# Optimization experiments

Hardware: AMD Instinct MI355X
Metric: run time of the kernel (lower is better)

Reference implementation:

```python
import jax, jax.numpy as jnp
import numpy as np

B, T, C = 4, 4096, 128

def setup_inputs() -> dict:
    key = jax.random.key(0)
    k1, k2, k3, k4 = jax.random.split(key, 4)
    x = jax.random.normal(k1, (B, T, C), dtype=jnp.float32)
    s = 1.0 / np.sqrt(C)
    Wq = jax.random.normal(k2, (C, C), dtype=jnp.float32) * s
    Wk = jax.random.normal(k3, (C, C), dtype=jnp.float32) * s
    Wv = jax.random.normal(k4, (C, C), dtype=jnp.float32) * s
    return {"x": x, "Wq": Wq, "Wk": Wk, "Wv": Wv}

def reference(x, Wq, Wk, Wv):
    # nn.Linear(bias=False): y = x @ W.T
    q = jnp.einsum('btc,dc->btd', x, Wq)
    k = jnp.einsum('btc,dc->btd', x, Wk)
    v = jnp.einsum('btc,dc->btd', x, Wv)
    scale = 1.0 / jnp.sqrt(jnp.asarray(x.shape[-1], x.dtype))
    att = jnp.einsum('btd,bsd->bts', q, k) * scale  # [B,T,T]
    causal = jnp.tril(jnp.ones((x.shape[1], x.shape[1]), dtype=bool))
    att = jnp.where(causal[None, :, :], att, -jnp.inf)
    w = jax.nn.softmax(att, axis=-1)
    # dropout p=0.0 -> identity
    out = jnp.einsum('bts,bsd->btd', w, v)
    return out
```

## Files before the change

### kernel.cpp

```cpp
#include <hip/hip_runtime.h>
#include <hip/hip_bf16.h>
#include <math.h>

#define T_SEQ 4096
#define C_DIM 128
#define B_SZ  4

typedef __attribute__((ext_vector_type(8))) short short8;
typedef __attribute__((ext_vector_type(4))) short short4v;
typedef __attribute__((ext_vector_type(4))) float f32x4;

__device__ __forceinline__ short f2bf(float f) {
    union { float fv; unsigned u; } v; v.fv = f;
    unsigned r = v.u + 0x7fff + ((v.u >> 16) & 1);
    return (short)(r >> 16);
}

__device__ __forceinline__ unsigned pk_bf16(float a, float b) {
    union { __hip_bfloat162 h2; unsigned u; } c;
    c.h2 = __float22bfloat162_rn(make_float2(a, b));
    return c.u;
}

__device__ __forceinline__ short8 load_f32x8_bf16(const float* p) {
    const float4* q = (const float4*)p;
    float4 a = q[0], b = q[1];
    short8 r;
    r[0] = f2bf(a.x); r[1] = f2bf(a.y); r[2] = f2bf(a.z); r[3] = f2bf(a.w);
    r[4] = f2bf(b.x); r[5] = f2bf(b.y); r[6] = f2bf(b.z); r[7] = f2bf(b.w);
    return r;
}

__device__ __forceinline__ void async_cp16(const short* g, short* l) {
    __builtin_amdgcn_global_load_lds(
        (const __attribute__((address_space(1))) unsigned int*)g,
        (__attribute__((address_space(3))) unsigned int*)l, 16, 0, 0);
}

__global__ __launch_bounds__(256) void qkv_proj(
    const float* __restrict__ x, const float* __restrict__ Wq,
    const float* __restrict__ Wk, const float* __restrict__ Wv,
    short* __restrict__ Q, short* __restrict__ Kf, short* __restrict__ Vf)
{
    __shared__ short8 Wl[2048];

    const int tid  = threadIdx.x;
    const int lane = tid & 63;
    const int ln15 = lane & 15;
    const int quad = lane >> 4;
    const int mat  = blockIdx.x >> 7;
    const int rt   = (blockIdx.x & 127) * 4 + (tid >> 6);
    const int m0   = rt * 32;

    const float* W = (mat == 0) ? Wq : (mat == 1) ? Wk : Wv;

#pragma unroll
    for (int it = 0; it < 8; ++it) {
        int i = tid + it * 256;
        int n = i >> 4, kc = i & 15;
        short8 v = load_f32x8_bf16(W + n * C_DIM + kc * 8);
        Wl[((n >> 4) * 4 + (kc >> 2)) * 64 + (kc & 3) * 16 + (n & 15)] = v;
    }

    short8 afr[2][4];
#pragma unroll
    for (int ms = 0; ms < 2; ++ms) {
        const float* xrow = x + (size_t)(m0 + ms * 16 + ln15) * C_DIM + quad * 8;
#pragma unroll
        for (int ks = 0; ks < 4; ++ks)
            afr[ms][ks] = load_f32x8_bf16(xrow + ks * 32);
    }

    __syncthreads();

    const float scale = (mat == 0) ? (0.08838834764831845f * 1.4426950408889634f)
                                   : 1.0f;
    const int b  = m0 >> 12;
    const int tl = m0 & 4095;

#pragma unroll
    for (int nt = 0; nt < 8; ++nt) {
        f32x4 acc0 = {0.f, 0.f, 0.f, 0.f};
        f32x4 acc1 = {0.f, 0.f, 0.f, 0.f};
#pragma unroll
        for (int ks = 0; ks < 4; ++ks) {
            short8 bfr = Wl[(nt * 4 + ks) * 64 + lane];
            if (mat == 2) {
                acc0 = __builtin_amdgcn_mfma_f32_16x16x32_bf16(afr[0][ks], bfr, acc0, 0, 0, 0);
                acc1 = __builtin_amdgcn_mfma_f32_16x16x32_bf16(afr[1][ks], bfr, acc1, 0, 0, 0);
            } else {
                acc0 = __builtin_amdgcn_mfma_f32_16x16x32_bf16(bfr, afr[0][ks], acc0, 0, 0, 0);
                acc1 = __builtin_amdgcn_mfma_f32_16x16x32_bf16(bfr, afr[1][ks], acc1, 0, 0, 0);
            }
        }
        if (mat == 0) {
            short4v s0, s1;
#pragma unroll
            for (int r = 0; r < 4; ++r) { s0[r] = f2bf(acc0[r] * scale); s1[r] = f2bf(acc1[r] * scale); }
            *(short4v*)&Q[(size_t)(m0 + ln15) * C_DIM + nt * 16 + quad * 4]      = s0;
            *(short4v*)&Q[(size_t)(m0 + 16 + ln15) * C_DIM + nt * 16 + quad * 4] = s1;
        } else if (mat == 1) {
            short4v s0, s1;
#pragma unroll
            for (int r = 0; r < 4; ++r) { s0[r] = f2bf(acc0[r]); s1[r] = f2bf(acc1[r]); }
            const int ks     = nt >> 1;
            const int quad_k = (nt & 1) * 2 + (quad >> 1);
            const int j0     = (quad & 1) * 4;
            {
                const int A0 = (tl >> 4) & 3;
                const int rd = tl >> 6;
                const int kt = (A0 >> 1) * 2 + ((ln15 >> 2) & 1);
                const int ar = (((A0 & 1) << 1) | ((ln15 >> 3) & 1)) * 4 + (ln15 & 3);
                size_t a = ((size_t)b << 19) + (size_t)rd * 8192
                         + (kt * 4 + ks) * 512 + quad_k * 128 + ar * 8 + j0;
                *(short4v*)&Kf[a] = s0;
            }
            {
                const int A1 = ((tl >> 4) + 1) & 3;
                const int rd = (tl + 16) >> 6;
                const int kt = (A1 >> 1) * 2 + ((ln15 >> 2) & 1);
                const int ar = (((A1 & 1) << 1) | ((ln15 >> 3) & 1)) * 4 + (ln15 & 3);
                size_t a = ((size_t)b << 19) + (size_t)rd * 8192
                         + (kt * 4 + ks) * 512 + quad_k * 128 + ar * 8 + j0;
                *(short4v*)&Kf[a] = s1;
            }
        } else {
            const int kvc = tl >> 5;
            short4v s0, s1;
#pragma unroll
            for (int r = 0; r < 4; ++r) { s0[r] = f2bf(acc0[r]); s1[r] = f2bf(acc1[r]); }
            short* vbase = Vf + (((size_t)(b * 128 + kvc) * 8 + nt) << 9);
            *(short4v*)&vbase[((quad >> 1) * 16 + ln15) * 8 + (quad & 1) * 4]       = s0;
            *(short4v*)&vbase[(((quad >> 1) + 2) * 16 + ln15) * 8 + (quad & 1) * 4] = s1;
        }
    }
}


#define QK8(KARR, SA, SB)                                                    \
    _Pragma("unroll")                                                        \
    for (int ks = 0; ks < 4; ++ks) {                                         \
      SA = __builtin_amdgcn_mfma_f32_16x16x32_bf16(KARR[ks],   qf[ks], SA, 0,0,0); \
      SB = __builtin_amdgcn_mfma_f32_16x16x32_bf16(KARR[4+ks], qf[ks], SB, 0,0,0); \
    }

#define SM8(SA, SB, PA)                                                      \
    {                                                                        \
      float p0 = __builtin_amdgcn_exp2f(SA[0] - 16.f);                       \
      float p1 = __builtin_amdgcn_exp2f(SA[1] - 16.f);                       \
      float p2 = __builtin_amdgcn_exp2f(SA[2] - 16.f);                       \
      float p3 = __builtin_amdgcn_exp2f(SA[3] - 16.f);                       \
      float p4 = __builtin_amdgcn_exp2f(SB[0] - 16.f);                       \
      float p5 = __builtin_amdgcn_exp2f(SB[1] - 16.f);                       \
      float p6 = __builtin_amdgcn_exp2f(SB[2] - 16.f);                       \
      float p7 = __builtin_amdgcn_exp2f(SB[3] - 16.f);                       \
      l_i += ((p0 + p1) + (p2 + p3)) + ((p4 + p5) + (p6 + p7));              \
      PA.u[0] = pk_bf16(p0, p1); PA.u[1] = pk_bf16(p2, p3);                  \
      PA.u[2] = pk_bf16(p4, p5); PA.u[3] = pk_bf16(p6, p7);                  \
    }

#define MASK8(SA, SB, CC)                                                    \
    if (32 * (CC) + 31 > Rw) {                                               \
      const int qcol = Rw + ln15;                                            \
      const int kb   = 32 * (CC) + quad * 8;                                 \
      _Pragma("unroll")                                                      \
      for (int rr = 0; rr < 4; ++rr) {                                       \
        if (kb + rr > qcol)     SA[rr] = -INFINITY;                          \
        if (kb + 4 + rr > qcol) SB[rr] = -INFINITY;                          \
      }                                                                      \
    }

#define PV8(VB_, OFF, PA)                                                    \
    _Pragma("unroll")                                                        \
    for (int dt = 0; dt < 8; ++dt) {                                         \
      short8 vfr = *(const short8*)&(VB_)[(OFF) + dt * 512 + lane * 8];      \
      acc[dt] = __builtin_amdgcn_mfma_f32_16x16x32_bf16(PA.s8, vfr,          \
                                                        acc[dt], 0, 0, 0);   \
    }

#define CHUNK2(KB_, VB_, T0)                                                 \
  {                                                                          \
    const int cc1 = qq + 4 * (T0) + 4;                                       \
    short8 kfr0[8];                                                          \
    _Pragma("unroll")                                                        \
    for (int j = 0; j < 8; ++j)                                              \
      kfr0[j] = *(const short8*)&(KB_)[j * 512 + lane * 8];                  \
    __builtin_amdgcn_s_setprio(1);                                           \
    f32x4 Sa0 = {0.f,0.f,0.f,0.f}, Sb0 = {0.f,0.f,0.f,0.f};                  \
    QK8(kfr0, Sa0, Sb0)                                                      \
    short8 kfr1[8];                                                          \
    _Pragma("unroll")                                                        \
    for (int j = 0; j < 8; ++j)                                              \
      kfr1[j] = *(const short8*)&(KB_)[4096 + j * 512 + lane * 8];           \
    f32x4 Sa1 = {0.f,0.f,0.f,0.f}, Sb1 = {0.f,0.f,0.f,0.f};                  \
    QK8(kfr1, Sa1, Sb1)                                                      \
    union { unsigned u[4]; short8 s8; } pa0, pa1;                            \
    SM8(Sa0, Sb0, pa0)                                                       \
    PV8(VB_, 0, pa0)                                                         \
    MASK8(Sa1, Sb1, cc1)                                                     \
    SM8(Sa1, Sb1, pa1)                                                       \
    PV8(VB_, 4096, pa1)                                                      \
    __builtin_amdgcn_s_setprio(0);                                           \
  }

#define CHUNK1(KB_, VB_, T0)                                                 \
  {                                                                          \
    const int cc0 = qq + 4 * (T0);                                           \
    short8 kfr0[8];                                                          \
    _Pragma("unroll")                                                        \
    for (int j = 0; j < 8; ++j)                                              \
      kfr0[j] = *(const short8*)&(KB_)[j * 512 + lane * 8];                  \
    __builtin_amdgcn_s_setprio(1);                                           \
    f32x4 Sa0 = {0.f,0.f,0.f,0.f}, Sb0 = {0.f,0.f,0.f,0.f};                  \
    QK8(kfr0, Sa0, Sb0)                                                      \
    MASK8(Sa0, Sb0, cc0)                                                     \
    union { unsigned u[4]; short8 s8; } pa0;                                 \
    SM8(Sa0, Sb0, pa0)                                                       \
    PV8(VB_, 0, pa0)                                                         \
    __builtin_amdgcn_s_setprio(0);                                           \
  }

#define ROUND(KC, VC, KN, VN, R)                                             \
  {                                                                          \
                       \
    asm volatile("s_waitcnt vmcnt(0)" ::: "memory");                         \
    __builtin_amdgcn_sched_barrier(0);                                       \
    __builtin_amdgcn_s_barrier();                                            \
    __builtin_amdgcn_sched_barrier(0);                                       \
          \
    {                                                                        \
      const int slot = (w >> 1) & 1;                                         \
      const int tS   = 2 * (R) + 2 + slot;                                   \
      if (tS <= gg) {                                                        \
        const int hw = w & 1;                                                \
        const short* src = ((w < 4) ? Kb : Vb)                               \
                         + (size_t)(qq + 4 * tS) * 4096 + hw * 2048;         \
        short* dst = ((w < 4) ? (KN) : (VN)) + slot * 4096 + hw * 2048;      \
        _Pragma("unroll")                                                    \
        for (int i = 0; i < 4; ++i)                                          \
          async_cp16(src + i * 512 + lane * 8, dst + i * 512);               \
      }                                                                      \
    }                                                                        \
    const int t0 = 2 * (R);                                                  \
    const bool a1 = (t0 + 1 <= gg) && (32 * (qq + 4 * t0 + 4) <= Rw + 15);   \
    const bool a0 = (t0 <= gg) && (32 * (qq + 4 * t0) <= Rw + 15);           \
    if (a1)      CHUNK2(KC, VC, t0)                                          \
    else if (a0) CHUNK1(KC, VC, t0)                                          \
  }

__global__ __launch_bounds__(512, 2) void flash_attn(
    const short* __restrict__ Q, const short* __restrict__ Kf,
    const short* __restrict__ Vf, float* __restrict__ part,
    float* __restrict__ lpart)
{
    __shared__ short Kld0[8192];
    __shared__ short Kld1[8192];
    __shared__ short Vld0[8192];
    __shared__ short Vld1[8192];

    const int tid  = threadIdx.x;
    const int w    = tid >> 6;
    const int lane = tid & 63;
    const int ln15 = lane & 15;
    const int quad = lane >> 4;
    const int bid  = blockIdx.x;

    const int u     = bid & 255;
    const int ph    = bid >> 8;
    const int xg    = u >> 3;
    const int gg    = ph ? xg : (31 - xg);
    const int combo = (ph << 3) | (u & 7);
    const int b     = combo >> 2;
    const int qq    = combo & 3;

    const int Rw   = 128 * gg + 16 * w;
    const int nrounds = (gg >> 1) + 1;

    const short* Qb = Q  + ((size_t)b << 19);
    const short* Kb = Kf + ((size_t)b << 19);
    const short* Vb = Vf + ((size_t)b << 19);

    short8 qf[4];
    {
        const short* qrow = Qb + (size_t)(Rw + ln15) * C_DIM + quad * 8;
#pragma unroll
        for (int ks = 0; ks < 4; ++ks)
            qf[ks] = *(const short8*)(qrow + ks * 32);
    }

    f32x4 acc[8];
#pragma unroll
    for (int dt = 0; dt < 8; ++dt)
        acc[dt] = (f32x4){0.f, 0.f, 0.f, 0.f};
    float l_i = 0.f;

    {
        const int slot = (w >> 1) & 1;
        const int tS   = slot;
        if (tS <= gg) {
            const int hw = w & 1;
            const short* src = ((w < 4) ? Kb : Vb)
                             + (size_t)(qq + 4 * tS) * 4096 + hw * 2048;
            short* dst = ((w < 4) ? Kld0 : Vld0) + slot * 4096 + hw * 2048;
#pragma unroll
            for (int i = 0; i < 4; ++i)
                async_cp16(src + i * 512 + lane * 8, dst + i * 512);
        }
    }

    int r = 0;
    while (true) {
        ROUND(Kld0, Vld0, Kld1, Vld1, r);
        if (++r >= nrounds) break;
        ROUND(Kld1, Vld1, Kld0, Vld0, r);
        if (++r >= nrounds) break;
    }

    l_i += __shfl_xor(l_i, 16);
    l_i += __shfl_xor(l_i, 32);

    float* pp = part + (((size_t)(qq * 4 + b)) * 4096 + Rw) * 128;
#pragma unroll
    for (int dt = 0; dt < 8; ++dt)
#pragma unroll
        for (int rr = 0; rr < 4; ++rr)
            pp[(quad * 4 + rr) * 128 + dt * 16 + ln15] = acc[dt][rr];
    if (quad == 0)
        lpart[(size_t)(qq * 4 + b) * 4096 + Rw + ln15] = l_i;
}

__global__ __launch_bounds__(256) void combine(
    const float* __restrict__ part, const float* __restrict__ lpart,
    float* __restrict__ out)
{
    const int tid = threadIdx.x;
    const int bid = blockIdx.x;

#pragma unroll
    for (int i = 0; i < 8; ++i) {
        int f4  = bid * 2048 + i * 256 + tid;
        int c4  = f4 & 31;
        int row = f4 >> 5;
        int b   = row >> 12;
        int trow = row & 4095;

        float4 p = make_float4(0.f, 0.f, 0.f, 0.f);
        float  l = 0.f;
#pragma unroll
        for (int q = 0; q < 4; ++q) {
            size_t base = (((size_t)(q * 4 + b)) * 4096 + trow) * 128 + c4 * 4;
            float4 pq = *(const float4*)&part[base];
            p.x += pq.x; p.y += pq.y; p.z += pq.z; p.w += pq.w;
            l += lpart[(size_t)(q * 4 + b) * 4096 + trow];
        }
        float li = 1.0f / l;
        float4 v;
        v.x = p.x * li; v.y = p.y * li; v.z = p.z * li; v.w = p.w * li;
        ((float4*)out)[f4] = v;
    }
}

extern "C" void kernel_launch(void* const* d_in, const int* in_sizes, int n_in,
                              void* d_out, int out_size, void* d_ws, size_t ws_size,
                              hipStream_t stream) {
    const float* x  = (const float*)d_in[0];
    const float* Wq = (const float*)d_in[1];
    const float* Wk = (const float*)d_in[2];
    const float* Wv = (const float*)d_in[3];
    float* out = (float*)d_out;

    const size_t elems = (size_t)B_SZ * T_SEQ * C_DIM;
    short* Q  = (short*)d_ws;
    short* Kf = Q  + elems;
    short* Vf = Kf + elems;
    float* part  = (float*)(Vf + elems);
    float* lpart = part + (size_t)16 * 4096 * 128;

    hipLaunchKernelGGL(qkv_proj, dim3(384), dim3(256), 0, stream,
                       x, Wq, Wk, Wv, Q, Kf, Vf);
    hipLaunchKernelGGL(flash_attn, dim3(512), dim3(512), 0, stream,
                       Q, Kf, Vf, part, lpart);
    hipLaunchKernelGGL(combine, dim3(256), dim3(256), 0, stream,
                       part, lpart, out);
}
```

Before: 108.0 us.

## Have each wave process 32 query rows to reuse K/V fragments across two tiles

Block size drops from 8 waves to 4, and each wave now owns 32 query rows (two 16-row tiles) instead of 16. Every K and V fragment read from LDS feeds MFMAs for both tiles, which halves LDS read traffic per unit of compute. The async copy work is redistributed so 2 waves load K and 2 load V, each covering full 4096-element slots. In exchange, accumulator registers per wave double and there are fewer waves available to hide latency, which may hurt occupancy. Masking is now applied to both chunks instead of being selectively skipped.

```diff
diff --git a/kernel.cpp b/kernel.cpp
--- a/kernel.cpp
+++ b/kernel.cpp
@@ -137,14 +137,18 @@
 }
 
 
-#define QK8(KARR, SA, SB)                                                    \
-    _Pragma("unroll")                                                        \
-    for (int ks = 0; ks < 4; ++ks) {                                         \
-      SA = __builtin_amdgcn_mfma_f32_16x16x32_bf16(KARR[ks],   qf[ks], SA, 0,0,0); \
-      SB = __builtin_amdgcn_mfma_f32_16x16x32_bf16(KARR[4+ks], qf[ks], SB, 0,0,0); \
-    }
-
-#define SM8(SA, SB, PA)                                                      \
+#define MASKT(SA, SB, CC, RQ)                                                \
+    if (32 * (CC) + 31 > (RQ)) {                                             \
+      const int qcol = (RQ) + ln15;                                          \
+      const int kb   = 32 * (CC) + quad * 8;                                 \
+      _Pragma("unroll")                                                      \
+      for (int rr = 0; rr < 4; ++rr) {                                       \
+        if (kb + rr > qcol)     SA[rr] = -INFINITY;                          \
+        if (kb + 4 + rr > qcol) SB[rr] = -INFINITY;                          \
+      }                                                                      \
+    }
+
+#define SM8(SA, SB, PA, LI)                                                  \
     {                                                                        \
       float p0 = __builtin_amdgcn_exp2f(SA[0] - 16.f);                       \
       float p1 = __builtin_amdgcn_exp2f(SA[1] - 16.f);                       \
@@ -154,69 +158,39 @@
       float p5 = __builtin_amdgcn_exp2f(SB[1] - 16.f);                       \
       float p6 = __builtin_amdgcn_exp2f(SB[2] - 16.f);                       \
       float p7 = __builtin_amdgcn_exp2f(SB[3] - 16.f);                       \
-      l_i += ((p0 + p1) + (p2 + p3)) + ((p4 + p5) + (p6 + p7));              \
+      LI += ((p0 + p1) + (p2 + p3)) + ((p4 + p5) + (p6 + p7));               \
       PA.u[0] = pk_bf16(p0, p1); PA.u[1] = pk_bf16(p2, p3);                  \
       PA.u[2] = pk_bf16(p4, p5); PA.u[3] = pk_bf16(p6, p7);                  \
     }
 
-#define MASK8(SA, SB, CC)                                                    \
-    if (32 * (CC) + 31 > Rw) {                                               \
-      const int qcol = Rw + ln15;                                            \
-      const int kb   = 32 * (CC) + quad * 8;                                 \
-      _Pragma("unroll")                                                      \
-      for (int rr = 0; rr < 4; ++rr) {                                       \
-        if (kb + rr > qcol)     SA[rr] = -INFINITY;                          \
-        if (kb + 4 + rr > qcol) SB[rr] = -INFINITY;                          \
-      }                                                                      \
-    }
-
-#define PV8(VB_, OFF, PA)                                                    \
+#define CHUNKW(KB_, VB_, S, T)                                               \
+  if ((T) <= gg && 32 * (qq + 4 * (T)) <= Rw + 31) {                         \
+    const int cc = qq + 4 * (T);                                             \
+    short8 kfr[8];                                                           \
+    _Pragma("unroll")                                                        \
+    for (int j = 0; j < 8; ++j)                                              \
+      kfr[j] = *(const short8*)&(KB_)[(S) * 4096 + j * 512 + lane * 8];      \
+    __builtin_amdgcn_s_setprio(1);                                           \
+    f32x4 Sa0 = {0.f,0.f,0.f,0.f}, Sb0 = {0.f,0.f,0.f,0.f};                  \
+    f32x4 Sa1 = {0.f,0.f,0.f,0.f}, Sb1 = {0.f,0.f,0.f,0.f};                  \
+    _Pragma("unroll")                                                        \
+    for (int ks = 0; ks < 4; ++ks) {                                         \
+      Sa0 = __builtin_amdgcn_mfma_f32_16x16x32_bf16(kfr[ks],   qf0[ks], Sa0, 0,0,0); \
+      Sb0 = __builtin_amdgcn_mfma_f32_16x16x32_bf16(kfr[4+ks], qf0[ks], Sb0, 0,0,0); \
+      Sa1 = __builtin_amdgcn_mfma_f32_16x16x32_bf16(kfr[ks],   qf1[ks], Sa1, 0,0,0); \
+      Sb1 = __builtin_amdgcn_mfma_f32_16x16x32_bf16(kfr[4+ks], qf1[ks], Sb1, 0,0,0); \
+    }                                                                        \
+    MASKT(Sa0, Sb0, cc, Rw)                                                  \
+    MASKT(Sa1, Sb1, cc, Rw + 16)                                             \
+    union { unsigned u[4]; short8 s8; } pa0, pa1;                            \
+    SM8(Sa0, Sb0, pa0, l0)                                                   \
+    SM8(Sa1, Sb1, pa1, l1)                                                   \
     _Pragma("unroll")                                                        \
     for (int dt = 0; dt < 8; ++dt) {                                         \
-      short8 vfr = *(const short8*)&(VB_)[(OFF) + dt * 512 + lane * 8];      \
-      acc[dt] = __builtin_amdgcn_mfma_f32_16x16x32_bf16(PA.s8, vfr,          \
-                                                        acc[dt], 0, 0, 0);   \
-    }
-
-#define CHUNK2(KB_, VB_, T0)                                                 \
-  {                                                                          \
-    const int cc1 = qq + 4 * (T0) + 4;                                       \
-    short8 kfr0[8];                                                          \
-    _Pragma("unroll")                                                        \
-    for (int j = 0; j < 8; ++j)                                              \
-      kfr0[j] = *(const short8*)&(KB_)[j * 512 + lane * 8];                  \
-    __builtin_amdgcn_s_setprio(1);                                           \
-    f32x4 Sa0 = {0.f,0.f,0.f,0.f}, Sb0 = {0.f,0.f,0.f,0.f};                  \
-    QK8(kfr0, Sa0, Sb0)                                                      \
-    short8 kfr1[8];                                                          \
-    _Pragma("unroll")                                                        \
-    for (int j = 0; j < 8; ++j)                                              \
-      kfr1[j] = *(const short8*)&(KB_)[4096 + j * 512 + lane * 8];           \
-    f32x4 Sa1 = {0.f,0.f,0.f,0.f}, Sb1 = {0.f,0.f,0.f,0.f};                  \
-    QK8(kfr1, Sa1, Sb1)                                                      \
-    union { unsigned u[4]; short8 s8; } pa0, pa1;                            \
-    SM8(Sa0, Sb0, pa0)                                                       \
-    PV8(VB_, 0, pa0)                                                         \
-    MASK8(Sa1, Sb1, cc1)                                                     \
-    SM8(Sa1, Sb1, pa1)                                                       \
-    PV8(VB_, 4096, pa1)                                                      \
-    __builtin_amdgcn_s_setprio(0);                                           \
-  }
-
-#define CHUNK1(KB_, VB_, T0)                                                 \
-  {                                                                          \
-    const int cc0 = qq + 4 * (T0);                                           \
-    short8 kfr0[8];                                                          \
-    _Pragma("unroll")                                                        \
-    for (int j = 0; j < 8; ++j)                                              \
-      kfr0[j] = *(const short8*)&(KB_)[j * 512 + lane * 8];                  \
-    __builtin_amdgcn_s_setprio(1);                                           \
-    f32x4 Sa0 = {0.f,0.f,0.f,0.f}, Sb0 = {0.f,0.f,0.f,0.f};                  \
-    QK8(kfr0, Sa0, Sb0)                                                      \
-    MASK8(Sa0, Sb0, cc0)                                                     \
-    union { unsigned u[4]; short8 s8; } pa0;                                 \
-    SM8(Sa0, Sb0, pa0)                                                       \
-    PV8(VB_, 0, pa0)                                                         \
+      short8 vfr = *(const short8*)&(VB_)[(S) * 4096 + dt * 512 + lane * 8]; \
+      acc0[dt] = __builtin_amdgcn_mfma_f32_16x16x32_bf16(pa0.s8, vfr, acc0[dt], 0,0,0); \
+      acc1[dt] = __builtin_amdgcn_mfma_f32_16x16x32_bf16(pa1.s8, vfr, acc1[dt], 0,0,0); \
+    }                                                                        \
     __builtin_amdgcn_s_setprio(0);                                           \
   }
 
@@ -227,28 +201,24 @@
     __builtin_amdgcn_sched_barrier(0);                                       \
     __builtin_amdgcn_s_barrier();                                            \
     __builtin_amdgcn_sched_barrier(0);                                       \
-          \
+                  \
     {                                                                        \
-      const int slot = (w >> 1) & 1;                                         \
+      const int slot = w & 1;                                                \
       const int tS   = 2 * (R) + 2 + slot;                                   \
       if (tS <= gg) {                                                        \
-        const int hw = w & 1;                                                \
-        const short* src = ((w < 4) ? Kb : Vb)                               \
-                         + (size_t)(qq + 4 * tS) * 4096 + hw * 2048;         \
-        short* dst = ((w < 4) ? (KN) : (VN)) + slot * 4096 + hw * 2048;      \
+        const short* src = ((w < 2) ? Kb : Vb)                               \
+                         + (size_t)(qq + 4 * tS) * 4096;                     \
+        short* dst = ((w < 2) ? (KN) : (VN)) + slot * 4096;                  \
         _Pragma("unroll")                                                    \
-        for (int i = 0; i < 4; ++i)                                          \
+        for (int i = 0; i < 8; ++i)                                          \
           async_cp16(src + i * 512 + lane * 8, dst + i * 512);               \
       }                                                                      \
     }                                                                        \
-    const int t0 = 2 * (R);                                                  \
-    const bool a1 = (t0 + 1 <= gg) && (32 * (qq + 4 * t0 + 4) <= Rw + 15);   \
-    const bool a0 = (t0 <= gg) && (32 * (qq + 4 * t0) <= Rw + 15);           \
-    if (a1)      CHUNK2(KC, VC, t0)                                          \
-    else if (a0) CHUNK1(KC, VC, t0)                                          \
+    CHUNKW(KC, VC, 0, 2 * (R))                                               \
+    CHUNKW(KC, VC, 1, 2 * (R) + 1)                                           \
   }
 
-__global__ __launch_bounds__(512, 2) void flash_attn(
+__global__ __launch_bounds__(256, 2) void flash_attn(
     const short* __restrict__ Q, const short* __restrict__ Kf,
     const short* __restrict__ Vf, float* __restrict__ part,
     float* __restrict__ lpart)
@@ -273,37 +243,41 @@
     const int b     = combo >> 2;
     const int qq    = combo & 3;
 
-    const int Rw   = 128 * gg + 16 * w;
+    const int Rw   = 128 * gg + 32 * w;
     const int nrounds = (gg >> 1) + 1;
 
     const short* Qb = Q  + ((size_t)b << 19);
     const short* Kb = Kf + ((size_t)b << 19);
     const short* Vb = Vf + ((size_t)b << 19);
 
-    short8 qf[4];
+    short8 qf0[4], qf1[4];
     {
-        const short* qrow = Qb + (size_t)(Rw + ln15) * C_DIM + quad * 8;
-#pragma unroll
-        for (int ks = 0; ks < 4; ++ks)
-            qf[ks] = *(const short8*)(qrow + ks * 32);
-    }
-
-    f32x4 acc[8];
-#pragma unroll
-    for (int dt = 0; dt < 8; ++dt)
-        acc[dt] = (f32x4){0.f, 0.f, 0.f, 0.f};
-    float l_i = 0.f;
+        const short* q0r = Qb + (size_t)(Rw + ln15) * C_DIM + quad * 8;
+        const short* q1r = Qb + (size_t)(Rw + 16 + ln15) * C_DIM + quad * 8;
+#pragma unroll
+        for (int ks = 0; ks < 4; ++ks) {
+            qf0[ks] = *(const short8*)(q0r + ks * 32);
+            qf1[ks] = *(const short8*)(q1r + ks * 32);
+        }
+    }
+
+    f32x4 acc0[8], acc1[8];
+#pragma unroll
+    for (int dt = 0; dt < 8; ++dt) {
+        acc0[dt] = (f32x4){0.f, 0.f, 0.f, 0.f};
+        acc1[dt] = (f32x4){0.f, 0.f, 0.f, 0.f};
+    }
+    float l0 = 0.f, l1 = 0.f;
 
     {
-        const int slot = (w >> 1) & 1;
+        const int slot = w & 1;
         const int tS   = slot;
         if (tS <= gg) {
-            const int hw = w & 1;
-            const short* src = ((w < 4) ? Kb : Vb)
-                             + (size_t)(qq + 4 * tS) * 4096 + hw * 2048;
-            short* dst = ((w < 4) ? Kld0 : Vld0) + slot * 4096 + hw * 2048;
-#pragma unroll
-            for (int i = 0; i < 4; ++i)
+            const short* src = ((w < 2) ? Kb : Vb)
+                             + (size_t)(qq + 4 * tS) * 4096;
+            short* dst = ((w < 2) ? Kld0 : Vld0) + slot * 4096;
+#pragma unroll
+            for (int i = 0; i < 8; ++i)
                 async_cp16(src + i * 512 + lane * 8, dst + i * 512);
         }
     }
@@ -316,17 +290,23 @@
         if (++r >= nrounds) break;
     }
 
-    l_i += __shfl_xor(l_i, 16);
-    l_i += __shfl_xor(l_i, 32);
+    l0 += __shfl_xor(l0, 16);
+    l0 += __shfl_xor(l0, 32);
+    l1 += __shfl_xor(l1, 16);
+    l1 += __shfl_xor(l1, 32);
 
     float* pp = part + (((size_t)(qq * 4 + b)) * 4096 + Rw) * 128;
 #pragma unroll
     for (int dt = 0; dt < 8; ++dt)
 #pragma unroll
-        for (int rr = 0; rr < 4; ++rr)
-            pp[(quad * 4 + rr) * 128 + dt * 16 + ln15] = acc[dt][rr];
-    if (quad == 0)
-        lpart[(size_t)(qq * 4 + b) * 4096 + Rw + ln15] = l_i;
+        for (int rr = 0; rr < 4; ++rr) {
+            pp[(quad * 4 + rr) * 128 + dt * 16 + ln15]        = acc0[dt][rr];
+            pp[(16 + quad * 4 + rr) * 128 + dt * 16 + ln15]   = acc1[dt][rr];
+        }
+    if (quad == 0) {
+        lpart[(size_t)(qq * 4 + b) * 4096 + Rw + ln15]      = l0;
+        lpart[(size_t)(qq * 4 + b) * 4096 + Rw + 16 + ln15] = l1;
+    }
 }
 
 __global__ __launch_bounds__(256) void combine(
@@ -378,7 +358,7 @@
 
     hipLaunchKernelGGL(qkv_proj, dim3(384), dim3(256), 0, stream,
                        x, Wq, Wk, Wv, Q, Kf, Vf);
-    hipLaunchKernelGGL(flash_attn, dim3(512), dim3(512), 0, stream,
+    hipLaunchKernelGGL(flash_attn, dim3(512), dim3(256), 0, stream,
                        Q, Kf, Vf, part, lpart);
     hipLaunchKernelGGL(combine, dim3(256), dim3(256), 0, stream,
                        part, lpart, out);
```

Result: slower. 112.9 us (+4.6%).

## Fuse split-KV combine into attention kernel via last-block atomic counter

Applied to the files above, without the earlier changes.

Removes the separate combine kernel launch. Each attention block writes its partial output and row sums, then atomically increments a per-(query tile, batch) counter. The fourth block to arrive reduces the four partials and writes the normalized output. The counters are zeroed in the projection kernel. This saves one launch and lets the reduction overlap other blocks' attention work, at the cost of a fence, an atomic and a tail reduction on the last-arriving blocks.

```diff
diff --git a/kernel.cpp b/kernel.cpp
--- a/kernel.cpp
+++ b/kernel.cpp
@@ -40,7 +40,8 @@
 __global__ __launch_bounds__(256) void qkv_proj(
     const float* __restrict__ x, const float* __restrict__ Wq,
     const float* __restrict__ Wk, const float* __restrict__ Wv,
-    short* __restrict__ Q, short* __restrict__ Kf, short* __restrict__ Vf)
+    short* __restrict__ Q, short* __restrict__ Kf, short* __restrict__ Vf,
+    unsigned* __restrict__ cnt)
 {
     __shared__ short8 Wl[2048];
 
@@ -51,6 +52,8 @@
     const int mat  = blockIdx.x >> 7;
     const int rt   = (blockIdx.x & 127) * 4 + (tid >> 6);
     const int m0   = rt * 32;
+
+    if (blockIdx.x == 0 && tid < 128) cnt[tid] = 0u;
 
     const float* W = (mat == 0) ? Wq : (mat == 1) ? Wk : Wv;
 
@@ -251,12 +254,14 @@
 __global__ __launch_bounds__(512, 2) void flash_attn(
     const short* __restrict__ Q, const short* __restrict__ Kf,
     const short* __restrict__ Vf, float* __restrict__ part,
-    float* __restrict__ lpart)
+    float* __restrict__ lpart, float* __restrict__ out,
+    unsigned* __restrict__ cnt)
 {
     __shared__ short Kld0[8192];
     __shared__ short Kld1[8192];
     __shared__ short Vld0[8192];
     __shared__ short Vld1[8192];
+    __shared__ unsigned lastflag;
 
     const int tid  = threadIdx.x;
     const int w    = tid >> 6;
@@ -327,36 +332,35 @@
             pp[(quad * 4 + rr) * 128 + dt * 16 + ln15] = acc[dt][rr];
     if (quad == 0)
         lpart[(size_t)(qq * 4 + b) * 4096 + Rw + ln15] = l_i;
-}
-
-__global__ __launch_bounds__(256) void combine(
-    const float* __restrict__ part, const float* __restrict__ lpart,
-    float* __restrict__ out)
-{
-    const int tid = threadIdx.x;
-    const int bid = blockIdx.x;
-
-#pragma unroll
-    for (int i = 0; i < 8; ++i) {
-        int f4  = bid * 2048 + i * 256 + tid;
-        int c4  = f4 & 31;
-        int row = f4 >> 5;
-        int b   = row >> 12;
-        int trow = row & 4095;
-
-        float4 p = make_float4(0.f, 0.f, 0.f, 0.f);
-        float  l = 0.f;
-#pragma unroll
-        for (int q = 0; q < 4; ++q) {
-            size_t base = (((size_t)(q * 4 + b)) * 4096 + trow) * 128 + c4 * 4;
-            float4 pq = *(const float4*)&part[base];
-            p.x += pq.x; p.y += pq.y; p.z += pq.z; p.w += pq.w;
-            l += lpart[(size_t)(q * 4 + b) * 4096 + trow];
+
+    __threadfence();
+    __syncthreads();
+    if (tid == 0)
+        lastflag = atomicAdd(&cnt[gg * 4 + b], 1u);
+    __syncthreads();
+    if (lastflag == 3u) {
+        __threadfence();
+        float* outb = out + ((size_t)b << 19);
+#pragma unroll
+        for (int i = 0; i < 8; ++i) {
+            int f4   = i * 512 + tid;
+            int c4   = f4 & 31;
+            int rloc = f4 >> 5;
+            int trow = gg * 128 + rloc;
+            float4 p = make_float4(0.f, 0.f, 0.f, 0.f);
+            float  l = 0.f;
+#pragma unroll
+            for (int q = 0; q < 4; ++q) {
+                size_t base = (((size_t)(q * 4 + b)) * 4096 + trow) * 128 + c4 * 4;
+                float4 pq = *(const float4*)&part[base];
+                p.x += pq.x; p.y += pq.y; p.z += pq.z; p.w += pq.w;
+                l += lpart[(size_t)(q * 4 + b) * 4096 + trow];
+            }
+            float li = 1.0f / l;
+            float4 v;
+            v.x = p.x * li; v.y = p.y * li; v.z = p.z * li; v.w = p.w * li;
+            *(float4*)&outb[(size_t)trow * 128 + c4 * 4] = v;
         }
-        float li = 1.0f / l;
-        float4 v;
-        v.x = p.x * li; v.y = p.y * li; v.z = p.z * li; v.w = p.w * li;
-        ((float4*)out)[f4] = v;
     }
 }
 
@@ -375,11 +379,10 @@
     short* Vf = Kf + elems;
     float* part  = (float*)(Vf + elems);
     float* lpart = part + (size_t)16 * 4096 * 128;
+    unsigned* cnt = (unsigned*)(lpart + (size_t)16 * 4096);
 
     hipLaunchKernelGGL(qkv_proj, dim3(384), dim3(256), 0, stream,
-                       x, Wq, Wk, Wv, Q, Kf, Vf);
+                       x, Wq, Wk, Wv, Q, Kf, Vf, cnt);
     hipLaunchKernelGGL(flash_attn, dim3(512), dim3(512), 0, stream,
-                       Q, Kf, Vf, part, lpart);
-    hipLaunchKernelGGL(combine, dim3(256), dim3(256), 0, stream,
-                       part, lpart, out);
-}
+                       Q, Kf, Vf, part, lpart, out, cnt);
+}
```

Result: slower. 354.8 us (+228.6%).
